# Optimization experiments

Measured on AMD Instinct MI355X. Metric: run time of the kernel, lower is better.

Reference implementation:

```python
import math
import jax, jax.numpy as jnp
import numpy as np

C = 32        # per-head dim
N_HEAD = 8
C_IN = 128

def setup_inputs() -> dict:
    key = jax.random.key(0)
    ks = jax.random.split(key, 10)
    B, S = 1, 256
    sc = 0.05  # keep logits in a sane range
    x    = jax.random.normal(ks[0], (B, S, S, C_IN), dtype=jnp.float32)
    bias = jax.random.normal(ks[1], (B, N_HEAD, S, S), dtype=jnp.float32)
    attention_mask = jax.random.randint(ks[2], (B, S, S), 0, 2).astype(bool)
    Wq = jax.random.normal(ks[3], (C_IN, C * N_HEAD), dtype=jnp.float32) * sc
    Wk = jax.random.normal(ks[4], (C_IN, C * N_HEAD), dtype=jnp.float32) * sc
    Wv = jax.random.normal(ks[5], (C_IN, C * N_HEAD), dtype=jnp.float32) * sc
    Wo = jax.random.normal(ks[6], (C * N_HEAD, C_IN), dtype=jnp.float32) * sc
    bo = jnp.zeros((C_IN,), dtype=jnp.float32)
    Wg = jax.random.normal(ks[7], (C_IN, C * N_HEAD), dtype=jnp.float32) * sc
    bg = jnp.zeros((C * N_HEAD,), dtype=jnp.float32)
    return {"x": x, "bias": bias, "attention_mask": attention_mask,
            "Wq": Wq, "Wk": Wk, "Wv": Wv, "Wo": Wo, "bo": bo, "Wg": Wg, "bg": bg}

def reference(x, bias, attention_mask, Wq, Wk, Wv, Wo, bo, Wg, bg):
    # x: [B, S, L, c_in]; attn_dim=2 is already the second-to-last dim,
    # so the torch movedim(attn_dim, -2) is the identity here.
    B, S, L, _ = x.shape
    q = x @ Wq  # [B, S, L, H*c]
    k = x @ Wk
    v = x @ Wv
    # split heads: [B, S, L, H, c] -> [B, S, H, L, c]
    def split_heads(t):
        return t.reshape(B, S, L, N_HEAD, C).transpose(0, 1, 3, 2, 4)
    q, k, v = split_heads(q), split_heads(k), split_heads(v)
    q = q / math.sqrt(C)
    # attention logits: [B, S, H, q, k]
    a = jnp.einsum('bshqc,bshkc->bshqk', q, k)
    # bias [B, H, q, k] -> broadcast over the axial batch dim S
    a = a + bias[:, None, :, :, :]
    # mask [B, S, k] -> [B, S, 1, 1, k]; masked positions get -inf
    m = attention_mask[:, :, None, None, :]
    a = jnp.where(m, a, -jnp.inf)
    a = jax.nn.softmax(a, axis=-1)
    o = jnp.einsum('bshqk,bshkc->bshqc', a, v)
    # merge heads: [B, S, H, L, c] -> [B, S, L, H*c]
    o = o.transpose(0, 1, 3, 2, 4).reshape(B, S, L, N_HEAD * C)
    # sigmoid gate
    g = jax.nn.sigmoid(x @ Wg + bg)
    o = g * o
    return o @ Wo + bo
```

## Files before the change

### kernel.cpp

```cpp
#include <hip/hip_runtime.h>
#include <hip/hip_bf16.h>
#include <cstdint>

#define CIN 128
#define NH 8
#define CH 32
#define LDQ16 1024

typedef short bf16x8 __attribute__((ext_vector_type(8)));
typedef float f32x4 __attribute__((ext_vector_type(4)));

__device__ __forceinline__ short f2bf(float f) {
  union { float f; unsigned u; } v; v.f = f;
  unsigned r = (v.u + 0x7FFFu + ((v.u >> 16) & 1u)) >> 16;
  return (short)r;
}
__device__ __forceinline__ float bf2f(short s) {
  union { unsigned u; float f; } v; v.u = ((unsigned)(unsigned short)s) << 16;
  return v.f;
}
__device__ __forceinline__ unsigned pk2bf(float a, float b) {
  union { __hip_bfloat162 h; unsigned u; } cv;
  cv.h = __float22bfloat162_rn(make_float2(a, b));
  return cv.u;
}

__global__ __launch_bounds__(256) void prep(
    const float* __restrict__ x,
    const float* __restrict__ Wq, const float* __restrict__ Wk,
    const float* __restrict__ Wv, const float* __restrict__ Wg,
    const float* __restrict__ Wo,
    const uint4* __restrict__ mask,
    short* __restrict__ xb, short* __restrict__ WT, short* __restrict__ WoT,
    unsigned int* __restrict__ flag)
{
  __shared__ int viol;
  const int b = blockIdx.x;
  if (b < 4096) {
    int base = (b * 256 + threadIdx.x) * 8;
    float4 a = *(const float4*)(x + base);
    float4 c = *(const float4*)(x + base + 4);
    bf16x8 r;
    r[0] = f2bf(a.x); r[1] = f2bf(a.y); r[2] = f2bf(a.z); r[3] = f2bf(a.w);
    r[4] = f2bf(c.x); r[5] = f2bf(c.y); r[6] = f2bf(c.z); r[7] = f2bf(c.w);
    *(bf16x8*)(xb + base) = r;
  } else if (b < 4160) {
    const float qscale = 0.17677669529663689f;
    int bb = b - 4096;
#pragma unroll
    for (int e = 0; e < 10; ++e) {
      int o = bb * 2560 + e * 256 + threadIdx.x;
      if (o < 131072) {
        int n = o >> 7, k = o & 127;
        int seg = n >> 8, nn = n & 255;
        const float* W = (seg == 0) ? Wq : (seg == 1) ? Wk : (seg == 2) ? Wv : Wg;
        float v = W[k * 256 + nn];
        if (seg == 0) v *= qscale;
        WT[o] = f2bf(v);
      } else {
        int o2 = o - 131072;
        int n = o2 >> 8, k = o2 & 255;
        WoT[o2] = f2bf(Wo[k * 128 + n]);
      }
    }
  } else {
    if (threadIdx.x == 0) viol = 0;
    __syncthreads();
    int v = 0;
#pragma unroll
    for (int j = 0; j < 16; ++j) {
      uint4 w = mask[j * 256 + threadIdx.x];
      v |= (w.x > 1u) | (w.y > 1u) | (w.z > 1u) | (w.w > 1u);
    }
    if (v) atomicOr(&viol, 1);
    __syncthreads();
    if (threadIdx.x == 0) *flag = viol ? 0u : 1u;
  }
}

__global__ __launch_bounds__(256) void proj_qkvg(
    const short* __restrict__ xb, const short* __restrict__ WT,
    const float* __restrict__ bg, short* __restrict__ qkvg)
{
  __shared__ short Al[64 * 136];
  __shared__ short Bl[128 * 136];
  const int tid = threadIdx.x;
  const int lane = tid & 63, w = tid >> 6;
  const int g = lane >> 4, c16 = lane & 15;
  const int wr = w & 1, wc = w >> 1;
  const int n0 = blockIdx.x * 128;
  const int row0 = blockIdx.y * 64;

  {
    const short* src = xb + (size_t)row0 * 128;
#pragma unroll
    for (int ch = 0; ch < 4; ++ch) {
      int c = ch * 256 + tid;
      int r = c >> 4, kc = c & 15;
      *(bf16x8*)&Al[r * 136 + kc * 8] = *(const bf16x8*)(src + r * 128 + kc * 8);
    }
    const short* wsrc = WT + (size_t)n0 * 128;
#pragma unroll
    for (int ch = 0; ch < 8; ++ch) {
      int c = ch * 256 + tid;
      int r = c >> 4, kc = c & 15;
      *(bf16x8*)&Bl[r * 136 + kc * 8] = *(const bf16x8*)(wsrc + r * 128 + kc * 8);
    }
  }
  __syncthreads();

  f32x4 acc[2][4];
#pragma unroll
  for (int rt = 0; rt < 2; ++rt)
#pragma unroll
    for (int ct = 0; ct < 4; ++ct) acc[rt][ct] = (f32x4){0.f, 0.f, 0.f, 0.f};

#pragma unroll
  for (int kk = 0; kk < 4; ++kk) {
    bf16x8 af[2], bfr[4];
#pragma unroll
    for (int rt = 0; rt < 2; ++rt)
      af[rt] = *(const bf16x8*)&Al[(wr * 32 + rt * 16 + c16) * 136 + kk * 32 + g * 8];
#pragma unroll
    for (int ct = 0; ct < 4; ++ct)
      bfr[ct] = *(const bf16x8*)&Bl[(wc * 64 + ct * 16 + c16) * 136 + kk * 32 + g * 8];
#pragma unroll
    for (int rt = 0; rt < 2; ++rt)
#pragma unroll
      for (int ct = 0; ct < 4; ++ct)
        acc[rt][ct] = __builtin_amdgcn_mfma_f32_16x16x32_bf16(af[rt], bfr[ct], acc[rt][ct], 0, 0, 0);
  }

  const int seg3 = (n0 >= 768);
  float bgv[4];
  if (seg3) {
#pragma unroll
    for (int ct = 0; ct < 4; ++ct)
      bgv[ct] = bg[n0 - 768 + wc * 64 + ct * 16 + c16];
  }
#pragma unroll
  for (int rt = 0; rt < 2; ++rt)
#pragma unroll
    for (int ct = 0; ct < 4; ++ct) {
      int col = n0 + wc * 64 + ct * 16 + c16;
#pragma unroll
      for (int i = 0; i < 4; ++i) {
        int row = row0 + wr * 32 + rt * 16 + g * 4 + i;
        float v = acc[rt][ct][i];
        if (seg3) v = 1.f / (1.f + __expf(-(v + bgv[ct])));
        qkvg[(size_t)row * LDQ16 + col] = f2bf(v);
      }
    }
}

__global__ __launch_bounds__(256) void attn(
    short* __restrict__ qkvg, const float* __restrict__ bias,
    const void* __restrict__ maskraw, const unsigned int* __restrict__ flagp)
{
  __shared__ __align__(16) short lds16[29456];
  const int tid = threadIdx.x;
  const int h = blockIdx.x;
  const int srow = blockIdx.y;
  const int lane = tid & 63, w = tid >> 6;
  const int g = lane >> 4, c16 = lane & 15;
  short* rowbase = qkvg + (size_t)srow * (256 * LDQ16);
  unsigned int* vTd = (unsigned int*)&lds16[10240];
  float* lL = (float*)&lds16[28928];

  const unsigned int fl = *flagp;
  int mv = fl ? ((const int*)maskraw)[srow * 256 + tid]
              : (int)((const unsigned char*)maskraw)[srow * 256 + tid];
  unsigned long long bb = __ballot(mv != 0);
  unsigned int* scratch = (unsigned int*)&lds16[29440];
  if (lane == 0) {
    scratch[w * 2 + 0] = (unsigned int)bb;
    scratch[w * 2 + 1] = (unsigned int)(bb >> 32);
  }

#pragma unroll
  for (int it = 0; it < 2; ++it) {
    int c = it * 256 + tid;
    int kp = c >> 2, cv = c & 3;
    const short* p0 = rowbase + (size_t)(2 * kp) * LDQ16 + 256 + h * CH + cv * 8;
    bf16x8 k0 = *(const bf16x8*)p0;
    bf16x8 k1 = *(const bf16x8*)(p0 + LDQ16);
    bf16x8 v0 = *(const bf16x8*)(p0 + 256);
    bf16x8 v1 = *(const bf16x8*)(p0 + LDQ16 + 256);
    *(bf16x8*)&lds16[(2 * kp) * 40 + cv * 8] = k0;
    *(bf16x8*)&lds16[(2 * kp + 1) * 40 + cv * 8] = k1;
#pragma unroll
    for (int j = 0; j < 8; ++j)
      vTd[(cv * 8 + j) * 132 + kp] =
          ((unsigned)(unsigned short)v0[j]) | (((unsigned)(unsigned short)v1[j]) << 16);
  }

  const int qb = w * 64;
  bf16x8 qf[4];
#pragma unroll
  for (int qt = 0; qt < 4; ++qt)
    qf[qt] = *(const bf16x8*)(rowbase + (size_t)(qb + qt * 16 + c16) * LDQ16 + h * CH + g * 8);

  __syncthreads();

  unsigned int mb[8];
#pragma unroll
  for (int j = 0; j < 8; ++j) mb[j] = scratch[j];

  const f32x4 zero4 = {0.f, 0.f, 0.f, 0.f};
  float l_[4] = {0.f, 0.f, 0.f, 0.f};
  f32x4 O[4][2];
#pragma unroll
  for (int qt = 0; qt < 4; ++qt) { O[qt][0] = zero4; O[qt][1] = zero4; }

  const int pbase = 18688 + w * 2560;
  const float* bh = bias + (size_t)h * 65536;

  for (int ch = 0; ch < 8; ++ch) {
    float4 bb4[2][4];
#pragma unroll
    for (int kt = 0; kt < 2; ++kt)
#pragma unroll
      for (int qt = 0; qt < 4; ++qt)
        bb4[kt][qt] = *(const float4*)(bh + (size_t)(qb + qt * 16 + c16) * 256 +
                                       ch * 32 + kt * 16 + g * 4);

#pragma unroll
    for (int kt = 0; kt < 2; ++kt) {
      bf16x8 kf = *(const bf16x8*)&lds16[(kt * 16 + c16) * 40 + g * 8];
      kf = *(const bf16x8*)&lds16[(ch * 32 + kt * 16 + c16) * 40 + g * 8];
      const unsigned nib = (mb[ch] >> (kt * 16 + g * 4)) & 0xFu;
      float em[4];
#pragma unroll
      for (int i = 0; i < 4; ++i) em[i] = ((nib >> i) & 1u) ? 1.f : 0.f;
#pragma unroll
      for (int qt = 0; qt < 4; ++qt) {
        f32x4 S = __builtin_amdgcn_mfma_f32_16x16x32_bf16(kf, qf[qt], zero4, 0, 0, 0);
        float p0 = em[0] * __expf(fminf(S[0] + bb4[kt][qt].x, 85.f));
        float p1 = em[1] * __expf(fminf(S[1] + bb4[kt][qt].y, 85.f));
        float p2 = em[2] * __expf(fminf(S[2] + bb4[kt][qt].z, 85.f));
        float p3 = em[3] * __expf(fminf(S[3] + bb4[kt][qt].w, 85.f));
        l_[qt] += (p0 + p1) + (p2 + p3);
        uint2 pw;
        pw.x = pk2bf(p0, p1);
        pw.y = pk2bf(p2, p3);
        *(uint2*)&lds16[pbase + (qt * 16 + c16) * 40 + kt * 16 + g * 4] = pw;
      }
    }
    bf16x8 vf0 = *(const bf16x8*)&vTd[(size_t)c16 * 132 + ch * 16 + g * 4];
    bf16x8 vf1 = *(const bf16x8*)&vTd[(size_t)(16 + c16) * 132 + ch * 16 + g * 4];
#pragma unroll
    for (int qt = 0; qt < 4; ++qt) {
      bf16x8 pf = *(const bf16x8*)&lds16[pbase + (qt * 16 + c16) * 40 + g * 8];
      O[qt][0] = __builtin_amdgcn_mfma_f32_16x16x32_bf16(pf, vf0, O[qt][0], 0, 0, 0);
      O[qt][1] = __builtin_amdgcn_mfma_f32_16x16x32_bf16(pf, vf1, O[qt][1], 0, 0, 0);
    }
  }

#pragma unroll
  for (int qt = 0; qt < 4; ++qt) {
    float v = l_[qt];
    v += __shfl_xor(v, 16);
    v += __shfl_xor(v, 32);
    if (lane < 16) lL[w * 64 + qt * 16 + c16] = v;
  }

#pragma unroll
  for (int qt = 0; qt < 4; ++qt)
#pragma unroll
    for (int i = 0; i < 4; ++i) {
      float l = lL[w * 64 + qt * 16 + g * 4 + i];
      float inv = 1.f / l;
      short* orow = rowbase + (size_t)(qb + qt * 16 + g * 4 + i) * LDQ16;
#pragma unroll
      for (int half = 0; half < 2; ++half) {
        int c = half * 16 + c16;
        float gv = bf2f(orow[768 + h * CH + c]);
        orow[h * CH + c] = f2bf(O[qt][half][i] * inv * gv);
      }
    }
}

__global__ __launch_bounds__(256) void out_proj(
    const short* __restrict__ og, const short* __restrict__ WoT,
    const float* __restrict__ bo, float* __restrict__ out)
{
  __shared__ short Al[64 * 136];
  __shared__ short Bl[128 * 136];
  const int tid = threadIdx.x;
  const int lane = tid & 63, w = tid >> 6;
  const int g = lane >> 4, c16 = lane & 15;
  const int wr = w & 1, wc = w >> 1;
  const int row0 = blockIdx.x * 64;

  f32x4 acc[2][4];
#pragma unroll
  for (int rt = 0; rt < 2; ++rt)
#pragma unroll
    for (int ct = 0; ct < 4; ++ct) acc[rt][ct] = (f32x4){0.f, 0.f, 0.f, 0.f};

  for (int kk0 = 0; kk0 < 256; kk0 += 128) {
#pragma unroll
    for (int ch = 0; ch < 4; ++ch) {
      int c = ch * 256 + tid;
      int r = c >> 4, kc = c & 15;
      *(bf16x8*)&Al[r * 136 + kc * 8] =
          *(const bf16x8*)(og + (size_t)(row0 + r) * LDQ16 + kk0 + kc * 8);
    }
#pragma unroll
    for (int ch = 0; ch < 8; ++ch) {
      int c = ch * 256 + tid;
      int r = c >> 4, kc = c & 15;
      *(bf16x8*)&Bl[r * 136 + kc * 8] =
          *(const bf16x8*)(WoT + (size_t)r * 256 + kk0 + kc * 8);
    }
    __syncthreads();
#pragma unroll
    for (int kk = 0; kk < 4; ++kk) {
      bf16x8 af[2], bfr[4];
#pragma unroll
      for (int rt = 0; rt < 2; ++rt)
        af[rt] = *(const bf16x8*)&Al[(wr * 32 + rt * 16 + c16) * 136 + kk * 32 + g * 8];
#pragma unroll
      for (int ct = 0; ct < 4; ++ct)
        bfr[ct] = *(const bf16x8*)&Bl[(wc * 64 + ct * 16 + c16) * 136 + kk * 32 + g * 8];
#pragma unroll
      for (int rt = 0; rt < 2; ++rt)
#pragma unroll
        for (int ct = 0; ct < 4; ++ct)
          acc[rt][ct] = __builtin_amdgcn_mfma_f32_16x16x32_bf16(af[rt], bfr[ct], acc[rt][ct], 0, 0, 0);
    }
    __syncthreads();
  }

#pragma unroll
  for (int rt = 0; rt < 2; ++rt)
#pragma unroll
    for (int ct = 0; ct < 4; ++ct) {
      int col = wc * 64 + ct * 16 + c16;
      float bv = bo[col];
#pragma unroll
      for (int i = 0; i < 4; ++i) {
        int row = row0 + wr * 32 + rt * 16 + g * 4 + i;
        out[(size_t)row * CIN + col] = acc[rt][ct][i] + bv;
      }
    }
}

extern "C" void kernel_launch(void* const* d_in, const int* in_sizes, int n_in,
                              void* d_out, int out_size, void* d_ws, size_t ws_size,
                              hipStream_t stream) {
  const float* x    = (const float*)d_in[0];
  const float* bias = (const float*)d_in[1];
  const void*  mask = d_in[2];
  const float* Wq   = (const float*)d_in[3];
  const float* Wk   = (const float*)d_in[4];
  const float* Wv   = (const float*)d_in[5];
  const float* Wo   = (const float*)d_in[6];
  const float* bo   = (const float*)d_in[7];
  const float* Wg   = (const float*)d_in[8];
  const float* bg   = (const float*)d_in[9];
  float* out = (float*)d_out;

  unsigned int* flag = (unsigned int*)d_ws;
  short* WT   = (short*)((char*)d_ws + 256);
  short* WoT  = WT + 131072;
  short* xb   = WoT + 32768;
  short* qkvg = xb + (size_t)65536 * 128;

  prep<<<4161, 256, 0, stream>>>(x, Wq, Wk, Wv, Wg, Wo, (const uint4*)mask,
                                 xb, WT, WoT, flag);
  proj_qkvg<<<dim3(8, 1024), 256, 0, stream>>>(xb, WT, bg, qkvg);
  attn<<<dim3(NH, 256), 256, 0, stream>>>(qkvg, bias, mask, flag);
  out_proj<<<1024, 256, 0, stream>>>(qkvg, WoT, bo, out);
}
```

Measured before the change: 274.7 us.

## Feed softmax probabilities to PV MFMA from registers, dropping LDS round-trip

Instead of writing the bf16 probabilities to a per-wave LDS tile and reading them back as MFMA operands, the kernel packs them straight into registers and runs 16x16x16 MFMAs against matching V fragments, one per key sub-tile. This removes the P staging buffer and frees LDS so more blocks fit per CU (launch bounds now request 4). The trade is twice as many smaller MFMA instructions and extra narrow V loads from LDS per sub-tile.

```diff
diff --git a/kernel.cpp b/kernel.cpp
--- a/kernel.cpp
+++ b/kernel.cpp
@@ -8,6 +8,7 @@
 #define LDQ16 1024
 
 typedef short bf16x8 __attribute__((ext_vector_type(8)));
+typedef short bf16x4 __attribute__((ext_vector_type(4)));
 typedef float f32x4 __attribute__((ext_vector_type(4)));
 
 __device__ __forceinline__ short f2bf(float f) {
@@ -153,11 +154,11 @@
     }
 }
 
-__global__ __launch_bounds__(256) void attn(
+__global__ __launch_bounds__(256, 4) void attn(
     short* __restrict__ qkvg, const float* __restrict__ bias,
     const void* __restrict__ maskraw, const unsigned int* __restrict__ flagp)
 {
-  __shared__ __align__(16) short lds16[29456];
+  __shared__ __align__(16) short lds16[19216];
   const int tid = threadIdx.x;
   const int h = blockIdx.x;
   const int srow = blockIdx.y;
@@ -165,13 +166,13 @@
   const int g = lane >> 4, c16 = lane & 15;
   short* rowbase = qkvg + (size_t)srow * (256 * LDQ16);
   unsigned int* vTd = (unsigned int*)&lds16[10240];
-  float* lL = (float*)&lds16[28928];
+  float* lL = (float*)&lds16[18688];
 
   const unsigned int fl = *flagp;
   int mv = fl ? ((const int*)maskraw)[srow * 256 + tid]
               : (int)((const unsigned char*)maskraw)[srow * 256 + tid];
   unsigned long long bb = __ballot(mv != 0);
-  unsigned int* scratch = (unsigned int*)&lds16[29440];
+  unsigned int* scratch = (unsigned int*)&lds16[19200];
   if (lane == 0) {
     scratch[w * 2 + 0] = (unsigned int)bb;
     scratch[w * 2 + 1] = (unsigned int)(bb >> 32);
@@ -212,7 +213,6 @@
 #pragma unroll
   for (int qt = 0; qt < 4; ++qt) { O[qt][0] = zero4; O[qt][1] = zero4; }
 
-  const int pbase = 18688 + w * 2560;
   const float* bh = bias + (size_t)h * 65536;
 
   for (int ch = 0; ch < 8; ++ch) {
@@ -226,8 +226,16 @@
 
 #pragma unroll
     for (int kt = 0; kt < 2; ++kt) {
-      bf16x8 kf = *(const bf16x8*)&lds16[(kt * 16 + c16) * 40 + g * 8];
-      kf = *(const bf16x8*)&lds16[(ch * 32 + kt * 16 + c16) * 40 + g * 8];
+      bf16x8 kf = *(const bf16x8*)&lds16[(ch * 32 + kt * 16 + c16) * 40 + g * 8];
+      bf16x4 vlo, vhi;
+      {
+        union { unsigned u[2]; bf16x4 v; } t0, t1;
+        const unsigned* plo = &vTd[(size_t)c16 * 132 + ch * 16 + kt * 8 + g * 2];
+        const unsigned* phi = &vTd[(size_t)(16 + c16) * 132 + ch * 16 + kt * 8 + g * 2];
+        t0.u[0] = plo[0]; t0.u[1] = plo[1];
+        t1.u[0] = phi[0]; t1.u[1] = phi[1];
+        vlo = t0.v; vhi = t1.v;
+      }
       const unsigned nib = (mb[ch] >> (kt * 16 + g * 4)) & 0xFu;
       float em[4];
 #pragma unroll
@@ -240,19 +248,12 @@
         float p2 = em[2] * __expf(fminf(S[2] + bb4[kt][qt].z, 85.f));
         float p3 = em[3] * __expf(fminf(S[3] + bb4[kt][qt].w, 85.f));
         l_[qt] += (p0 + p1) + (p2 + p3);
-        uint2 pw;
-        pw.x = pk2bf(p0, p1);
-        pw.y = pk2bf(p2, p3);
-        *(uint2*)&lds16[pbase + (qt * 16 + c16) * 40 + kt * 16 + g * 4] = pw;
-      }
-    }
-    bf16x8 vf0 = *(const bf16x8*)&vTd[(size_t)c16 * 132 + ch * 16 + g * 4];
-    bf16x8 vf1 = *(const bf16x8*)&vTd[(size_t)(16 + c16) * 132 + ch * 16 + g * 4];
-#pragma unroll
-    for (int qt = 0; qt < 4; ++qt) {
-      bf16x8 pf = *(const bf16x8*)&lds16[pbase + (qt * 16 + c16) * 40 + g * 8];
-      O[qt][0] = __builtin_amdgcn_mfma_f32_16x16x32_bf16(pf, vf0, O[qt][0], 0, 0, 0);
-      O[qt][1] = __builtin_amdgcn_mfma_f32_16x16x32_bf16(pf, vf1, O[qt][1], 0, 0, 0);
+        union { unsigned u[2]; bf16x4 v; } pu;
+        pu.u[0] = pk2bf(p0, p1);
+        pu.u[1] = pk2bf(p2, p3);
+        O[qt][0] = __builtin_amdgcn_mfma_f32_16x16x16bf16_1k(pu.v, vlo, O[qt][0], 0, 0, 0);
+        O[qt][1] = __builtin_amdgcn_mfma_f32_16x16x16bf16_1k(pu.v, vhi, O[qt][1], 0, 0, 0);
+      }
     }
   }
 
```

New measurement: 259.8 us. 5.4% less time.
